# Performance work log

Measured on AMD Instinct MI355X. Metric: run time of the kernel, lower is better.

The kernel has to match this reference:

```python
import jax, jax.numpy as jnp
import numpy as np

N, F, H, C, E = 100000, 128, 128, 32, 600000


def setup_inputs() -> dict:
    key = jax.random.key(0)
    ks = jax.random.split(key, 8)
    x = jax.random.normal(ks[0], (N, F), dtype=jnp.float32)
    edge_index = jax.random.randint(ks[1], (2, E), 0, N, dtype=jnp.int64)
    s = 1.0 / np.sqrt(F)
    sh = 1.0 / np.sqrt(H)
    W1l = jax.random.uniform(ks[2], (F, H), jnp.float32, -s, s)
    W1r = jax.random.uniform(ks[3], (F, H), jnp.float32, -s, s)
    b1 = jnp.zeros((H,), jnp.float32)
    W2l = jax.random.uniform(ks[4], (H, C), jnp.float32, -sh, sh)
    W2r = jax.random.uniform(ks[5], (H, C), jnp.float32, -sh, sh)
    b2 = jnp.zeros((C,), jnp.float32)
    return {"x": x, "edge_index": edge_index, "W1l": W1l, "b1": b1,
            "W1r": W1r, "W2l": W2l, "b2": b2, "W2r": W2r}


def reference(x, edge_index, W1l, b1, W1r, W2l, b2, W2r):
    # PyG SAGEConv: out = lin_l(mean_{j in N(i)} x_j) + lin_r(x_i)
    # (lin_l has bias, lin_r does not). Dropout is identity in eval mode.
    src, dst = edge_index[0], edge_index[1]
    n = x.shape[0]
    deg = jax.ops.segment_sum(jnp.ones((src.shape[0],), x.dtype), dst, num_segments=n)
    inv_deg = 1.0 / jnp.maximum(deg, 1.0)  # clamp: isolated nodes get 0 agg

    def sage(h, Wl, bl, Wr):
        agg = jax.ops.segment_sum(h[src], dst, num_segments=n)  # [N, d] gather+scatter
        agg = agg * inv_deg[:, None]
        return agg @ Wl + bl + h @ Wr

    h = jax.nn.relu(sage(x, W1l, b1, W1r))
    return sage(h, W2l, b2, W2r)
```

## Files before the change

kernel.cpp:

```cpp
#include <hip/hip_runtime.h>
#include <hip/hip_bf16.h>


#define FDIM 128
#define CDIM 32
#define SCAN_CHUNK 1024
#define PSTR 136

typedef __attribute__((ext_vector_type(8))) short short8;
typedef __attribute__((ext_vector_type(4))) float f32x4;
typedef unsigned short ushort_t;
typedef unsigned int uint_t;

static __device__ __forceinline__ ushort_t f2bf(float f) {
    uint_t u = __float_as_uint(f);
    u += 0x7fffu + ((u >> 16) & 1u);
    return (ushort_t)(u >> 16);
}
static __device__ __forceinline__ float bf2f_lo(uint_t u) {
    return __uint_as_float(u << 16);
}
static __device__ __forceinline__ float bf2f_hi(uint_t u) {
    return __uint_as_float(u & 0xffff0000u);
}


__global__ __launch_bounds__(256) void prep_kernel(
        const float* __restrict__ x, uint_t* __restrict__ xb4, long long total8,
        const int* __restrict__ dst, int* __restrict__ deg, int E, int n,
        const float* __restrict__ W1l, const float* __restrict__ W1r,
        const float* __restrict__ W2l, const float* __restrict__ W2r,
        ushort_t* __restrict__ w1lt, ushort_t* __restrict__ w1rt,
        ushort_t* __restrict__ w2lt, ushort_t* __restrict__ w2rt,
        int CB, int DB) {
    int b = (int)blockIdx.x;
    if (b < CB) {
        long long i = (long long)b * 256 + threadIdx.x;
        if (i >= total8) return;
        const float4* p = (const float4*)x + i * 2;
        float4 v0 = p[0], v1 = p[1];
        uint4 o;
        o.x = (uint_t)f2bf(v0.x) | ((uint_t)f2bf(v0.y) << 16);
        o.y = (uint_t)f2bf(v0.z) | ((uint_t)f2bf(v0.w) << 16);
        o.z = (uint_t)f2bf(v1.x) | ((uint_t)f2bf(v1.y) << 16);
        o.w = (uint_t)f2bf(v1.z) | ((uint_t)f2bf(v1.w) << 16);
        ((uint4*)xb4)[i] = o;
    } else if (b < CB + DB) {
        int e = (b - CB) * 256 + threadIdx.x;
        if (e < E) {
            int d = dst[e];
            if (d >= 0 && d < n) atomicAdd(&deg[d], 1);
        }
    } else {
        int idx = (b - CB - DB) * 256 + threadIdx.x;
        const float* w; ushort_t* wt; int Nc, local;
        if (idx < 16384)      { w = W1l; wt = w1lt; Nc = 128; local = idx; }
        else if (idx < 32768) { w = W1r; wt = w1rt; Nc = 128; local = idx - 16384; }
        else if (idx < 36864) { w = W2l; wt = w2lt; Nc = 32;  local = idx - 32768; }
        else if (idx < 40960) { w = W2r; wt = w2rt; Nc = 32;  local = idx - 36864; }
        else return;
        int nn = local >> 7, kk = local & 127;
        wt[nn * 128 + kk] = f2bf(w[kk * Nc + nn]);
    }
}


__global__ __launch_bounds__(256) void scan1_kernel(
        const int* __restrict__ deg, int* __restrict__ partials, int n) {
    __shared__ int red[256];
    int t = threadIdx.x;
    int base = blockIdx.x * SCAN_CHUNK + t * 4;
    int s = 0;
    if (base + 3 < n) {
        int4 v = *(const int4*)(deg + base);
        s = v.x + v.y + v.z + v.w;
    } else {
        for (int i = 0; i < 4; i++) if (base + i < n) s += deg[base + i];
    }
    red[t] = s;
    __syncthreads();
#pragma unroll
    for (int off = 128; off > 0; off >>= 1) {
        if (t < off) red[t] += red[t + off];
        __syncthreads();
    }
    if (t == 0) partials[blockIdx.x] = red[0];
}

__global__ __launch_bounds__(256) void scan3_kernel(
        const int* __restrict__ deg, const int* __restrict__ partials,
        int* __restrict__ rowptr, float* __restrict__ inv_deg, int n, int SB) {
    __shared__ int s[256];
    int t = threadIdx.x;
    int pre = (t < SB && t < (int)blockIdx.x) ? partials[t] : 0;
    s[t] = pre;
    __syncthreads();
#pragma unroll
    for (int off = 128; off > 0; off >>= 1) {
        if (t < off) s[t] += s[t + off];
        __syncthreads();
    }
    int blockbase = s[0];
    __syncthreads();

    int base = blockIdx.x * SCAN_CHUNK + t * 4;
    int d0 = 0, d1 = 0, d2 = 0, d3 = 0;
    if (base + 3 < n) {
        int4 v = *(const int4*)(deg + base);
        d0 = v.x; d1 = v.y; d2 = v.z; d3 = v.w;
    } else {
        if (base + 0 < n) d0 = deg[base + 0];
        if (base + 1 < n) d1 = deg[base + 1];
        if (base + 2 < n) d2 = deg[base + 2];
        if (base + 3 < n) d3 = deg[base + 3];
    }
    s[t] = d0 + d1 + d2 + d3;
    __syncthreads();
#pragma unroll
    for (int off = 1; off < 256; off <<= 1) {
        int u = (t >= off) ? s[t - off] : 0;
        __syncthreads();
        s[t] += u;
        __syncthreads();
    }
    int run = blockbase + ((t == 0) ? 0 : s[t - 1]);
    int dd[4] = {d0, d1, d2, d3};
#pragma unroll
    for (int i = 0; i < 4; i++) {
        if (base + i < n) {
            rowptr[base + i]  = run;
            inv_deg[base + i] = 1.0f / (float)(dd[i] > 0 ? dd[i] : 1);
            run += dd[i];
        }
    }
}

__global__ void fill_kernel(const int* __restrict__ src, const int* __restrict__ dst,
                            const int* __restrict__ rowptr, int* __restrict__ cursor,
                            int* __restrict__ nbr, int E, int n) {
    int e = blockIdx.x * 256 + threadIdx.x;
    if (e < E) {
        int s = src[e];
        int d = dst[e];
        if (d >= 0 && d < n) {
            int p = atomicAdd(&cursor[d], 1);
            nbr[rowptr[d] + p] = s;
        }
    }
}


__global__ __launch_bounds__(256) void agg1_kernel(
        const uint_t* __restrict__ xbu ,
        const int* __restrict__ rowptr, const int* __restrict__ deg,
        const int* __restrict__ nbr, const float* __restrict__ inv_deg,
        uint_t* __restrict__ aggbu, int n) {
    int t = threadIdx.x;
    int i = blockIdx.x * 4 + (t >> 6);
    if (i >= n) return;
    int lane = t & 63;
    int g    = lane >> 4;
    int l16  = lane & 15;
    int start = rowptr[i];
    int d     = deg[i];
    float s[8] = {0.f, 0.f, 0.f, 0.f, 0.f, 0.f, 0.f, 0.f};
    int e = g;
    for (; e + 4 < d; e += 8) {
        int j0 = nbr[start + e];
        int j1 = nbr[start + e + 4];
        uint4 u0 = *(const uint4*)(xbu + (size_t)j0 * 64 + l16 * 4);
        uint4 u1 = *(const uint4*)(xbu + (size_t)j1 * 64 + l16 * 4);
        s[0] += bf2f_lo(u0.x) + bf2f_lo(u1.x); s[1] += bf2f_hi(u0.x) + bf2f_hi(u1.x);
        s[2] += bf2f_lo(u0.y) + bf2f_lo(u1.y); s[3] += bf2f_hi(u0.y) + bf2f_hi(u1.y);
        s[4] += bf2f_lo(u0.z) + bf2f_lo(u1.z); s[5] += bf2f_hi(u0.z) + bf2f_hi(u1.z);
        s[6] += bf2f_lo(u0.w) + bf2f_lo(u1.w); s[7] += bf2f_hi(u0.w) + bf2f_hi(u1.w);
    }
    if (e < d) {
        int j = nbr[start + e];
        uint4 u = *(const uint4*)(xbu + (size_t)j * 64 + l16 * 4);
        s[0] += bf2f_lo(u.x); s[1] += bf2f_hi(u.x);
        s[2] += bf2f_lo(u.y); s[3] += bf2f_hi(u.y);
        s[4] += bf2f_lo(u.z); s[5] += bf2f_hi(u.z);
        s[6] += bf2f_lo(u.w); s[7] += bf2f_hi(u.w);
    }
#pragma unroll
    for (int k = 0; k < 8; k++) {
        s[k] += __shfl_xor(s[k], 16, 64);
        s[k] += __shfl_xor(s[k], 32, 64);
    }
    if (g == 0) {
        float inv = inv_deg[i];
        uint4 o;
        o.x = (uint_t)f2bf(s[0] * inv) | ((uint_t)f2bf(s[1] * inv) << 16);
        o.y = (uint_t)f2bf(s[2] * inv) | ((uint_t)f2bf(s[3] * inv) << 16);
        o.z = (uint_t)f2bf(s[4] * inv) | ((uint_t)f2bf(s[5] * inv) << 16);
        o.w = (uint_t)f2bf(s[6] * inv) | ((uint_t)f2bf(s[7] * inv) << 16);
        *(uint4*)(aggbu + (size_t)i * 64 + l16 * 4) = o;
    }
}


__global__ __launch_bounds__(512) void fused12_kernel(
        const ushort_t* __restrict__ xb, const ushort_t* __restrict__ aggb,
        const ushort_t* __restrict__ w1lt, const ushort_t* __restrict__ w1rt,
        const ushort_t* __restrict__ w2lt, const ushort_t* __restrict__ w2rt,
        const float* __restrict__ b1,
        ushort_t* __restrict__ z2b, float* __restrict__ r2, int n) {
    __shared__ ushort_t xs[64 * PSTR];
    __shared__ ushort_t as_[64 * PSTR];
    __shared__ ushort_t ws2[2 * 32 * PSTR];

    const int t    = threadIdx.x;
    const int wave = t >> 6;
    const int lane = t & 63;
    const int quad = lane >> 4;
    const int l16  = lane & 15;
    const int row0 = blockIdx.x * 64;
    const int c1   = wave * 16;

#pragma unroll
    for (int it = 0; it < 2; it++) {
        int c   = t + it * 512;
        int row = c >> 4, col = c & 15;
        int grow = row0 + row; if (grow >= n) grow = n - 1;
        size_t goff = (size_t)grow * FDIM + col * 8;
        short8 vx = *(const short8*)(xb + goff);
        short8 va = *(const short8*)(aggb + goff);
        *(short8*)(xs  + row * PSTR + col * 8) = vx;
        *(short8*)(as_ + row * PSTR + col * 8) = va;
    }
#pragma unroll
    for (int it = 0; it < 2; it++) {
        int c = t + it * 512;
        int m = c >> 9, lo = c & 511;
        int row = lo >> 4, col = lo & 15;
        const ushort_t* sw = m ? w2rt : w2lt;
        *(short8*)(ws2 + (m * 32 + row) * PSTR + col * 8) =
            *(const short8*)(sw + row * 128 + col * 8);
    }

    short8 bl1[4], br1[4];
#pragma unroll
    for (int k = 0; k < 4; k++) {
        size_t woff = (size_t)(c1 + l16) * FDIM + k * 32 + quad * 8;
        bl1[k] = *(const short8*)(w1lt + woff);
        br1[k] = *(const short8*)(w1rt + woff);
    }
    float b1c = b1[c1 + l16];

    __syncthreads();

    f32x4 acc1[4];
#pragma unroll
    for (int r = 0; r < 4; r++) acc1[r] = (f32x4){0.f, 0.f, 0.f, 0.f};

#pragma unroll
    for (int k = 0; k < 4; k++) {
        short8 a1[4], a2[4];
#pragma unroll
        for (int r = 0; r < 4; r++) {
            int lro = (r * 16 + l16) * PSTR + k * 32 + quad * 8;
            a1[r] = *(const short8*)(as_ + lro);
            a2[r] = *(const short8*)(xs  + lro);
        }
#pragma unroll
        for (int r = 0; r < 4; r++) {
            acc1[r] = __builtin_amdgcn_mfma_f32_16x16x32_bf16(a1[r], bl1[k], acc1[r], 0, 0, 0);
            acc1[r] = __builtin_amdgcn_mfma_f32_16x16x32_bf16(a2[r], br1[k], acc1[r], 0, 0, 0);
        }
    }

    __syncthreads();

    ushort_t* hs = xs;
#pragma unroll
    for (int r = 0; r < 4; r++)
#pragma unroll
        for (int reg = 0; reg < 4; reg++) {
            int lrow = r * 16 + quad * 4 + reg;
            float v = acc1[r][reg] + b1c;
            v = v > 0.f ? v : 0.f;
            hs[lrow * PSTR + c1 + l16] = f2bf(v);
        }

    __syncthreads();

    const int rs = (wave >> 1) * 16;
    const int c2 = (wave & 1) * 16;
    f32x4 a2l = (f32x4){0.f, 0.f, 0.f, 0.f};
    f32x4 a2r = (f32x4){0.f, 0.f, 0.f, 0.f};
#pragma unroll
    for (int k = 0; k < 4; k++) {
        short8 ah = *(const short8*)(hs  + (rs + l16) * PSTR + k * 32 + quad * 8);
        short8 wl = *(const short8*)(ws2 + (c2 + l16) * PSTR + k * 32 + quad * 8);
        short8 wr = *(const short8*)(ws2 + (32 + c2 + l16) * PSTR + k * 32 + quad * 8);
        a2l = __builtin_amdgcn_mfma_f32_16x16x32_bf16(ah, wl, a2l, 0, 0, 0);
        a2r = __builtin_amdgcn_mfma_f32_16x16x32_bf16(ah, wr, a2r, 0, 0, 0);
    }
#pragma unroll
    for (int reg = 0; reg < 4; reg++) {
        int grow = row0 + rs + quad * 4 + reg;
        if (grow < n) {
            z2b[(size_t)grow * CDIM + c2 + l16] = f2bf(a2l[reg]);
            r2 [(size_t)grow * CDIM + c2 + l16] = a2r[reg];
        }
    }
}


__global__ __launch_bounds__(256) void combine2_kernel(
        const uint_t* __restrict__ z2bu ,
        const int* __restrict__ rowptr, const int* __restrict__ deg,
        const int* __restrict__ nbr, const float* __restrict__ inv_deg,
        const float* __restrict__ b2, const float* __restrict__ r2,
        float* __restrict__ out, int n) {
    int t = threadIdx.x;
    int i = blockIdx.x * 4 + (t >> 6);
    if (i >= n) return;
    int lane = t & 63;
    int g    = lane >> 4;
    int l16  = lane & 15;
    int start = rowptr[i];
    int d     = deg[i];
    float s0 = 0.f, s1 = 0.f;
    int e = g;
    for (; e + 4 < d; e += 8) {
        int j0 = nbr[start + e];
        int j1 = nbr[start + e + 4];
        uint_t u0 = z2bu[(size_t)j0 * 16 + l16];
        uint_t u1 = z2bu[(size_t)j1 * 16 + l16];
        s0 += bf2f_lo(u0) + bf2f_lo(u1);
        s1 += bf2f_hi(u0) + bf2f_hi(u1);
    }
    if (e < d) {
        int j = nbr[start + e];
        uint_t u = z2bu[(size_t)j * 16 + l16];
        s0 += bf2f_lo(u);
        s1 += bf2f_hi(u);
    }
    s0 += __shfl_xor(s0, 16, 64); s0 += __shfl_xor(s0, 32, 64);
    s1 += __shfl_xor(s1, 16, 64); s1 += __shfl_xor(s1, 32, 64);
    if (g == 0) {
        float inv = inv_deg[i];
        float2 rr = *(const float2*)(r2 + (size_t)i * CDIM + l16 * 2);
        float2 o;
        o.x = s0 * inv + rr.x + b2[l16 * 2];
        o.y = s1 * inv + rr.y + b2[l16 * 2 + 1];
        *(float2*)(out + (size_t)i * CDIM + l16 * 2) = o;
    }
}


extern "C" void kernel_launch(void* const* d_in, const int* in_sizes, int n_in,
                              void* d_out, int out_size, void* d_ws, size_t ws_size,
                              hipStream_t stream) {
    const float* x   = (const float*)d_in[0];
    const int*   ei  = (const int*)d_in[1];
    const float* W1l = (const float*)d_in[2];
    const float* b1  = (const float*)d_in[3];
    const float* W1r = (const float*)d_in[4];
    const float* W2l = (const float*)d_in[5];
    const float* b2  = (const float*)d_in[6];
    const float* W2r = (const float*)d_in[7];

    const int N = in_sizes[0] / FDIM;
    const int E = in_sizes[1] / 2;
    const int* src = ei;
    const int* dst = ei + E;

    char* p = (char*)d_ws;
    int*      deg      = (int*)p;      p += (size_t)N * sizeof(int);
    int*      cursor   = (int*)p;      p += (size_t)N * sizeof(int);
    int*      rowptr   = (int*)p;      p += (size_t)N * sizeof(int);
    float*    inv_deg  = (float*)p;    p += (size_t)N * sizeof(float);
    int*      partials = (int*)p;      p += 256 * sizeof(int);
    ushort_t* w1lt     = (ushort_t*)p; p += FDIM * FDIM * sizeof(ushort_t);
    ushort_t* w1rt     = (ushort_t*)p; p += FDIM * FDIM * sizeof(ushort_t);
    ushort_t* w2lt     = (ushort_t*)p; p += FDIM * CDIM * sizeof(ushort_t);
    ushort_t* w2rt     = (ushort_t*)p; p += FDIM * CDIM * sizeof(ushort_t);
    int*      nbr      = (int*)p;      p += (size_t)((E + 3) / 4 * 4) * sizeof(int);
    ushort_t* xb       = (ushort_t*)p; p += (size_t)N * FDIM * sizeof(ushort_t);
    ushort_t* aggb     = (ushort_t*)p; p += (size_t)N * FDIM * sizeof(ushort_t);
    ushort_t* z2b      = (ushort_t*)p; p += (size_t)N * CDIM * sizeof(ushort_t);
    float*    r2       = (float*)p;    p += (size_t)N * CDIM * sizeof(float);

    const int SB = (N + SCAN_CHUNK - 1) / SCAN_CHUNK;
    const long long total8 = (long long)N * FDIM / 8;
    const int CB = (int)((total8 + 255) / 256);
    const int DB = (E + 255) / 256;
    const int WB = (40960 + 255) / 256;

    hipMemsetAsync(deg, 0, 2 * (size_t)N * sizeof(int), stream);

    prep_kernel <<<CB + DB + WB, 256, 0, stream>>>(x, (uint_t*)xb, total8, dst, deg, E, N,
                                                   W1l, W1r, W2l, W2r,
                                                   w1lt, w1rt, w2lt, w2rt, CB, DB);
    scan1_kernel<<<SB, 256, 0, stream>>>(deg, partials, N);
    scan3_kernel<<<SB, 256, 0, stream>>>(deg, partials, rowptr, inv_deg, N, SB);
    fill_kernel <<<DB, 256, 0, stream>>>(src, dst, rowptr, cursor, nbr, E, N);

    agg1_kernel   <<<(N + 3) / 4, 256, 0, stream>>>((const uint_t*)xb, rowptr, deg, nbr,
                                                    inv_deg, (uint_t*)aggb, N);
    fused12_kernel<<<(N + 63) / 64, 512, 0, stream>>>(xb, aggb, w1lt, w1rt, w2lt, w2rt,
                                                      b1, z2b, r2, N);
    combine2_kernel<<<(N + 3) / 4, 256, 0, stream>>>((const uint_t*)z2b, rowptr, deg, nbr,
                                                     inv_deg, b2, r2, (float*)d_out, N);
}
```

Baseline: 255.8 us.

## Split degree counting, compute inverse degree inline, widen combine2 lanes, bound fused12 occupancy

Moves the degree atomics out of prep_kernel into their own deg_kernel. It removes the inv_deg array and computes 1/deg inline in agg1 and combine2. combine2 now gives 8 lanes per neighbor with uint2 loads and float4 stores, so each pass of the loop covers more edges. fused12 gets a min-blocks-per-CU launch bound, which may cap its registers and cause spills. These are several unrelated small tweaks: the extra launch adds overhead, while the inv_deg stores and loads go away.

```diff
diff --git a/kernel.cpp b/kernel.cpp
--- a/kernel.cpp
+++ b/kernel.cpp
@@ -25,14 +25,23 @@
 }
 
 
+__global__ void deg_kernel(const int* __restrict__ dst, int* __restrict__ deg,
+                           int E, int n) {
+    int e = blockIdx.x * 256 + threadIdx.x;
+    if (e < E) {
+        int d = dst[e];
+        if (d >= 0 && d < n) atomicAdd(&deg[d], 1);
+    }
+}
+
+
 __global__ __launch_bounds__(256) void prep_kernel(
         const float* __restrict__ x, uint_t* __restrict__ xb4, long long total8,
-        const int* __restrict__ dst, int* __restrict__ deg, int E, int n,
         const float* __restrict__ W1l, const float* __restrict__ W1r,
         const float* __restrict__ W2l, const float* __restrict__ W2r,
         ushort_t* __restrict__ w1lt, ushort_t* __restrict__ w1rt,
         ushort_t* __restrict__ w2lt, ushort_t* __restrict__ w2rt,
-        int CB, int DB) {
+        int CB) {
     int b = (int)blockIdx.x;
     if (b < CB) {
         long long i = (long long)b * 256 + threadIdx.x;
@@ -45,14 +54,8 @@
         o.z = (uint_t)f2bf(v1.x) | ((uint_t)f2bf(v1.y) << 16);
         o.w = (uint_t)f2bf(v1.z) | ((uint_t)f2bf(v1.w) << 16);
         ((uint4*)xb4)[i] = o;
-    } else if (b < CB + DB) {
-        int e = (b - CB) * 256 + threadIdx.x;
-        if (e < E) {
-            int d = dst[e];
-            if (d >= 0 && d < n) atomicAdd(&deg[d], 1);
-        }
     } else {
-        int idx = (b - CB - DB) * 256 + threadIdx.x;
+        int idx = (b - CB) * 256 + threadIdx.x;
         const float* w; ushort_t* wt; int Nc, local;
         if (idx < 16384)      { w = W1l; wt = w1lt; Nc = 128; local = idx; }
         else if (idx < 32768) { w = W1r; wt = w1rt; Nc = 128; local = idx - 16384; }
@@ -89,7 +92,7 @@
 
 __global__ __launch_bounds__(256) void scan3_kernel(
         const int* __restrict__ deg, const int* __restrict__ partials,
-        int* __restrict__ rowptr, float* __restrict__ inv_deg, int n, int SB) {
+        int* __restrict__ rowptr, int n, int SB) {
     __shared__ int s[256];
     int t = threadIdx.x;
     int pre = (t < SB && t < (int)blockIdx.x) ? partials[t] : 0;
@@ -128,8 +131,7 @@
 #pragma unroll
     for (int i = 0; i < 4; i++) {
         if (base + i < n) {
-            rowptr[base + i]  = run;
-            inv_deg[base + i] = 1.0f / (float)(dd[i] > 0 ? dd[i] : 1);
+            rowptr[base + i] = run;
             run += dd[i];
         }
     }
@@ -153,8 +155,7 @@
 __global__ __launch_bounds__(256) void agg1_kernel(
         const uint_t* __restrict__ xbu ,
         const int* __restrict__ rowptr, const int* __restrict__ deg,
-        const int* __restrict__ nbr, const float* __restrict__ inv_deg,
-        uint_t* __restrict__ aggbu, int n) {
+        const int* __restrict__ nbr, uint_t* __restrict__ aggbu, int n) {
     int t = threadIdx.x;
     int i = blockIdx.x * 4 + (t >> 6);
     if (i >= n) return;
@@ -189,7 +190,7 @@
         s[k] += __shfl_xor(s[k], 32, 64);
     }
     if (g == 0) {
-        float inv = inv_deg[i];
+        float inv = 1.0f / (float)(d > 0 ? d : 1);
         uint4 o;
         o.x = (uint_t)f2bf(s[0] * inv) | ((uint_t)f2bf(s[1] * inv) << 16);
         o.y = (uint_t)f2bf(s[2] * inv) | ((uint_t)f2bf(s[3] * inv) << 16);
@@ -200,7 +201,7 @@
 }
 
 
-__global__ __launch_bounds__(512) void fused12_kernel(
+__global__ __launch_bounds__(512, 6) void fused12_kernel(
         const ushort_t* __restrict__ xb, const ushort_t* __restrict__ aggb,
         const ushort_t* __restrict__ w1lt, const ushort_t* __restrict__ w1rt,
         const ushort_t* __restrict__ w2lt, const ushort_t* __restrict__ w2rt,
@@ -311,42 +312,50 @@
 __global__ __launch_bounds__(256) void combine2_kernel(
         const uint_t* __restrict__ z2bu ,
         const int* __restrict__ rowptr, const int* __restrict__ deg,
-        const int* __restrict__ nbr, const float* __restrict__ inv_deg,
-        const float* __restrict__ b2, const float* __restrict__ r2,
-        float* __restrict__ out, int n) {
+        const int* __restrict__ nbr, const float* __restrict__ b2,
+        const float* __restrict__ r2, float* __restrict__ out, int n) {
     int t = threadIdx.x;
     int i = blockIdx.x * 4 + (t >> 6);
     if (i >= n) return;
     int lane = t & 63;
-    int g    = lane >> 4;
-    int l16  = lane & 15;
+    int sub  = lane >> 3;
+    int l8   = lane & 7;
     int start = rowptr[i];
     int d     = deg[i];
-    float s0 = 0.f, s1 = 0.f;
-    int e = g;
-    for (; e + 4 < d; e += 8) {
+    float s0 = 0.f, s1 = 0.f, s2 = 0.f, s3 = 0.f;
+    int e = sub;
+    for (; e + 8 < d; e += 16) {
         int j0 = nbr[start + e];
-        int j1 = nbr[start + e + 4];
-        uint_t u0 = z2bu[(size_t)j0 * 16 + l16];
-        uint_t u1 = z2bu[(size_t)j1 * 16 + l16];
-        s0 += bf2f_lo(u0) + bf2f_lo(u1);
-        s1 += bf2f_hi(u0) + bf2f_hi(u1);
+        int j1 = nbr[start + e + 8];
+        uint2 u0 = *(const uint2*)(z2bu + (size_t)j0 * 16 + l8 * 2);
+        uint2 u1 = *(const uint2*)(z2bu + (size_t)j1 * 16 + l8 * 2);
+        s0 += bf2f_lo(u0.x) + bf2f_lo(u1.x);
+        s1 += bf2f_hi(u0.x) + bf2f_hi(u1.x);
+        s2 += bf2f_lo(u0.y) + bf2f_lo(u1.y);
+        s3 += bf2f_hi(u0.y) + bf2f_hi(u1.y);
     }
     if (e < d) {
         int j = nbr[start + e];
-        uint_t u = z2bu[(size_t)j * 16 + l16];
-        s0 += bf2f_lo(u);
-        s1 += bf2f_hi(u);
-    }
-    s0 += __shfl_xor(s0, 16, 64); s0 += __shfl_xor(s0, 32, 64);
-    s1 += __shfl_xor(s1, 16, 64); s1 += __shfl_xor(s1, 32, 64);
-    if (g == 0) {
-        float inv = inv_deg[i];
-        float2 rr = *(const float2*)(r2 + (size_t)i * CDIM + l16 * 2);
-        float2 o;
-        o.x = s0 * inv + rr.x + b2[l16 * 2];
-        o.y = s1 * inv + rr.y + b2[l16 * 2 + 1];
-        *(float2*)(out + (size_t)i * CDIM + l16 * 2) = o;
+        uint2 u = *(const uint2*)(z2bu + (size_t)j * 16 + l8 * 2);
+        s0 += bf2f_lo(u.x);
+        s1 += bf2f_hi(u.x);
+        s2 += bf2f_lo(u.y);
+        s3 += bf2f_hi(u.y);
+    }
+    s0 += __shfl_xor(s0, 8, 64); s0 += __shfl_xor(s0, 16, 64); s0 += __shfl_xor(s0, 32, 64);
+    s1 += __shfl_xor(s1, 8, 64); s1 += __shfl_xor(s1, 16, 64); s1 += __shfl_xor(s1, 32, 64);
+    s2 += __shfl_xor(s2, 8, 64); s2 += __shfl_xor(s2, 16, 64); s2 += __shfl_xor(s2, 32, 64);
+    s3 += __shfl_xor(s3, 8, 64); s3 += __shfl_xor(s3, 16, 64); s3 += __shfl_xor(s3, 32, 64);
+    if (sub == 0) {
+        float inv = 1.0f / (float)(d > 0 ? d : 1);
+        float4 rr = *(const float4*)(r2 + (size_t)i * CDIM + l8 * 4);
+        float4 bb = *(const float4*)(b2 + l8 * 4);
+        float4 o;
+        o.x = s0 * inv + rr.x + bb.x;
+        o.y = s1 * inv + rr.y + bb.y;
+        o.z = s2 * inv + rr.z + bb.z;
+        o.w = s3 * inv + rr.w + bb.w;
+        *(float4*)(out + (size_t)i * CDIM + l8 * 4) = o;
     }
 }
 
@@ -372,7 +381,6 @@
     int*      deg      = (int*)p;      p += (size_t)N * sizeof(int);
     int*      cursor   = (int*)p;      p += (size_t)N * sizeof(int);
     int*      rowptr   = (int*)p;      p += (size_t)N * sizeof(int);
-    float*    inv_deg  = (float*)p;    p += (size_t)N * sizeof(float);
     int*      partials = (int*)p;      p += 256 * sizeof(int);
     ushort_t* w1lt     = (ushort_t*)p; p += FDIM * FDIM * sizeof(ushort_t);
     ushort_t* w1rt     = (ushort_t*)p; p += FDIM * FDIM * sizeof(ushort_t);
@@ -392,17 +400,18 @@
 
     hipMemsetAsync(deg, 0, 2 * (size_t)N * sizeof(int), stream);
 
-    prep_kernel <<<CB + DB + WB, 256, 0, stream>>>(x, (uint_t*)xb, total8, dst, deg, E, N,
-                                                   W1l, W1r, W2l, W2r,
-                                                   w1lt, w1rt, w2lt, w2rt, CB, DB);
+    prep_kernel <<<CB + WB, 256, 0, stream>>>(x, (uint_t*)xb, total8,
+                                              W1l, W1r, W2l, W2r,
+                                              w1lt, w1rt, w2lt, w2rt, CB);
+    deg_kernel  <<<DB, 256, 0, stream>>>(dst, deg, E, N);
     scan1_kernel<<<SB, 256, 0, stream>>>(deg, partials, N);
-    scan3_kernel<<<SB, 256, 0, stream>>>(deg, partials, rowptr, inv_deg, N, SB);
+    scan3_kernel<<<SB, 256, 0, stream>>>(deg, partials, rowptr, N, SB);
     fill_kernel <<<DB, 256, 0, stream>>>(src, dst, rowptr, cursor, nbr, E, N);
 
     agg1_kernel   <<<(N + 3) / 4, 256, 0, stream>>>((const uint_t*)xb, rowptr, deg, nbr,
-                                                    inv_deg, (uint_t*)aggb, N);
+                                                    (uint_t*)aggb, N);
     fused12_kernel<<<(N + 63) / 64, 512, 0, stream>>>(xb, aggb, w1lt, w1rt, w2lt, w2rt,
                                                       b1, z2b, r2, N);
     combine2_kernel<<<(N + 3) / 4, 256, 0, stream>>>((const uint_t*)z2b, rowptr, deg, nbr,
-                                                     inv_deg, b2, r2, (float*)d_out, N);
-}
+                                                     b2, r2, (float*)d_out, N);
+}
```

New measurement: 249.6 us. -2.4%, faster.
